# Kernel optimization log

Hardware: AMD Instinct MI355X
Metric: run time of the kernel (lower is better)

Reference implementation:

```python
import jax, jax.numpy as jnp
import numpy as np
from functools import partial

REG = 0.1
NUM_ITERS = 50
EPS_NORM = 1e-8
EPS_SINK = 1e-10


def _cdist(x0, x1):
    # torch.cdist(p=2): pairwise euclidean distance [B,N,N]
    sq0 = jnp.sum(x0 * x0, axis=-1)                     # [B,N]
    sq1 = jnp.sum(x1 * x1, axis=-1)                     # [B,N]
    inner = jnp.einsum('bnd,bmd->bnm', x0, x1)          # [B,N,N]
    d2 = sq0[:, :, None] + sq1[:, None, :] - 2.0 * inner
    return jnp.sqrt(jnp.maximum(d2, 0.0))


def setup_inputs() -> dict:
    key = jax.random.key(0)
    k0, k1 = jax.random.split(key)
    B, N, D = 8, 2048, 64
    x0 = jax.random.normal(k0, (B, N, D), dtype=jnp.float32)
    x1 = jax.random.normal(k1, (B, N, D), dtype=jnp.float32)
    return {"x0": x0, "x1": x1}


def reference(x0, x1):
    B, N, D = x0.shape
    # cost matrix + per-batch max normalization
    C = _cdist(x0, x1)
    C = C / (jnp.max(C, axis=(-2, -1), keepdims=True) + EPS_NORM)
    # Gibbs kernel
    K = jnp.exp(-C / REG)                               # [B,N,N]
    # Sinkhorn fixed-point iterations
    u0 = jnp.full((B, N), 1.0 / N, dtype=K.dtype)
    v0 = jnp.full((B, N), 1.0 / N, dtype=K.dtype)

    def body(i, uv):
        u, v = uv
        u = 1.0 / (jnp.einsum('bij,bj->bi', K, v) + EPS_SINK)
        v = 1.0 / (jnp.einsum('bij,bi->bj', K, u) + EPS_SINK)
        return (u, v)

    u, v = jax.lax.fori_loop(0, NUM_ITERS, body, (u0, v0))
    # transport plan P = diag(u) K diag(v)
    P = u[:, :, None] * K * v[:, None, :]               # [B,N,N]
    # greedy matching: argmax over columns
    matchings = jnp.argmax(P, axis=-1)                  # [B,N] int
    return matchings
```

## Files before the change

kernel.cpp:

```cpp
#include <hip/hip_runtime.h>
#include <hip/hip_bf16.h>
#include <stdint.h>

#define BB 8
#define NN 2048
#define DD 64
#define REGv 0.1f
#define NUM_ITERS 50
#define EPS_NORM 1e-8f
#define EPS_SINK 1e-10f
#define CHUNK 16
#define NBLK (NN / CHUNK)

__global__ void init_k(float* v, unsigned* maxd) {
    int t = blockIdx.x * 256 + threadIdx.x;
    if (t < BB * NN) v[t] = 1.0f / (float)NN;
    if (t < BB) maxd[t] = 0u;
}

__global__ void sq_k(const float* __restrict__ x0, const float* __restrict__ x1,
                     float* __restrict__ sq0, float* __restrict__ sq1) {
    int w = (blockIdx.x * 256 + threadIdx.x) >> 6;
    int lane = threadIdx.x & 63;
    if (w >= 2 * BB * NN) return;
    const float* src = (w < BB * NN) ? x0 : x1;
    int r = (w < BB * NN) ? w : w - BB * NN;
    float val = src[(size_t)r * DD + lane];
    float s = val * val;
    #pragma unroll
    for (int off = 32; off; off >>= 1) s += __shfl_xor(s, off);
    if (lane == 0) ((w < BB * NN) ? sq0 : sq1)[r] = s;
}

template<int WRITE>
__global__ __launch_bounds__(256) void distc_k(const float* __restrict__ x0,
                                               const float* __restrict__ x1,
                                               const float* __restrict__ sq0,
                                               const float* __restrict__ sq1,
                                               float* __restrict__ Kd,
                                               unsigned* __restrict__ maxd) {
    __shared__ float x0s[128 * 68];
    __shared__ float x1t[64 * 68];
    __shared__ float wred[4];
    int bid = blockIdx.x;
    int b = bid >> 9;
    int tile = bid & 511;
    int ti = tile >> 5, tj = tile & 31;
    int i0 = ti * 128, j0 = tj * 64;
    int t = threadIdx.x;

    const float4* g0 = (const float4*)(x0 + ((size_t)b * NN + i0) * DD);
    #pragma unroll
    for (int rep = 0; rep < 8; rep++) {
        int e = rep * 256 + t;
        int row = e >> 4, c4 = e & 15;
        *(float4*)&x0s[row * 68 + c4 * 4] = g0[row * 16 + c4];
    }
    const float4* g1 = (const float4*)(x1 + ((size_t)b * NN + j0) * DD);
    #pragma unroll
    for (int rep = 0; rep < 4; rep++) {
        int e = rep * 256 + t;
        int row = e >> 4, c4 = e & 15;
        float4 a = g1[row * 16 + c4];
        x1t[(c4 * 4 + 0) * 68 + row] = a.x;
        x1t[(c4 * 4 + 1) * 68 + row] = a.y;
        x1t[(c4 * 4 + 2) * 68 + row] = a.z;
        x1t[(c4 * 4 + 3) * 68 + row] = a.w;
    }
    __syncthreads();

    int tx = t & 15, ty = t >> 4;
    float4 acc4[8];
    #pragma unroll
    for (int di = 0; di < 8; di++) acc4[di] = make_float4(0.f, 0.f, 0.f, 0.f);

    #pragma unroll
    for (int k4 = 0; k4 < 16; k4++) {
        float4 b0 = *(const float4*)&x1t[(k4 * 4 + 0) * 68 + tx * 4];
        float4 b1 = *(const float4*)&x1t[(k4 * 4 + 1) * 68 + tx * 4];
        float4 b2 = *(const float4*)&x1t[(k4 * 4 + 2) * 68 + tx * 4];
        float4 b3 = *(const float4*)&x1t[(k4 * 4 + 3) * 68 + tx * 4];
        #pragma unroll
        for (int di = 0; di < 8; di++) {
            float4 a = *(const float4*)&x0s[(ty * 8 + di) * 68 + k4 * 4];
            acc4[di].x += a.x * b0.x + a.y * b1.x + a.z * b2.x + a.w * b3.x;
            acc4[di].y += a.x * b0.y + a.y * b1.y + a.z * b2.y + a.w * b3.y;
            acc4[di].z += a.x * b0.z + a.y * b1.z + a.z * b2.z + a.w * b3.z;
            acc4[di].w += a.x * b0.w + a.y * b1.w + a.z * b2.w + a.w * b3.w;
        }
    }

    int ib = b * NN + i0 + ty * 8;
    float4 s1 = *(const float4*)&sq1[b * NN + j0 + tx * 4];

    if (WRITE) {
        float mv = sqrtf(__uint_as_float(maxd[b])) + EPS_NORM;
        #pragma unroll
        for (int di = 0; di < 8; di++) {
            float s0 = sq0[ib + di];
            float4 o;
            o.x = expf(-((sqrtf(fmaxf(s0 + s1.x - 2.f * acc4[di].x, 0.f)) / mv) / REGv));
            o.y = expf(-((sqrtf(fmaxf(s0 + s1.y - 2.f * acc4[di].y, 0.f)) / mv) / REGv));
            o.z = expf(-((sqrtf(fmaxf(s0 + s1.z - 2.f * acc4[di].z, 0.f)) / mv) / REGv));
            o.w = expf(-((sqrtf(fmaxf(s0 + s1.w - 2.f * acc4[di].w, 0.f)) / mv) / REGv));
            *(float4*)&Kd[(size_t)(ib + di) * NN + j0 + tx * 4] = o;
        }
    } else {
        float lm = 0.0f;
        #pragma unroll
        for (int di = 0; di < 8; di++) {
            float s0 = sq0[ib + di];
            lm = fmaxf(lm, fmaxf(s0 + s1.x - 2.f * acc4[di].x, 0.f));
            lm = fmaxf(lm, fmaxf(s0 + s1.y - 2.f * acc4[di].y, 0.f));
            lm = fmaxf(lm, fmaxf(s0 + s1.z - 2.f * acc4[di].z, 0.f));
            lm = fmaxf(lm, fmaxf(s0 + s1.w - 2.f * acc4[di].w, 0.f));
        }
        #pragma unroll
        for (int off = 32; off; off >>= 1) lm = fmaxf(lm, __shfl_xor(lm, off));
        if ((t & 63) == 0) wred[t >> 6] = lm;
        __syncthreads();
        if (t == 0) {
            float m = fmaxf(fmaxf(wred[0], wred[1]), fmaxf(wred[2], wred[3]));
            atomicMax(&maxd[b], __float_as_uint(m));
        }
    }
}

__global__ __launch_bounds__(512) void sink_k(const float* __restrict__ Kd,
                                              const float* __restrict__ v,
                                              float* __restrict__ u,
                                              float* __restrict__ partial) {
    __shared__ float red[8][CHUNK];
    __shared__ float uu_s[CHUNK];
    int bid = blockIdx.x;
    int b = bid >> 7;
    int chunk = bid & 127;
    int row0 = chunk * CHUNK;
    int t = threadIdx.x;

    float4 vv = ((const float4*)(v + (size_t)b * NN))[t];
    const float4* Kr = (const float4*)(Kd + ((size_t)b * NN + row0) * NN);
    float4 kk[CHUNK];
    #pragma unroll
    for (int r = 0; r < CHUNK; r++) kk[r] = Kr[r * 512 + t];

    float dp[CHUNK];
    #pragma unroll
    for (int r = 0; r < CHUNK; r++)
        dp[r] = kk[r].x * vv.x + kk[r].y * vv.y + kk[r].z * vv.z + kk[r].w * vv.w;
    #pragma unroll
    for (int r = 0; r < CHUNK; r++)
        #pragma unroll
        for (int off = 32; off; off >>= 1) dp[r] += __shfl_xor(dp[r], off);
    int lane = t & 63, w = t >> 6;
    if (lane == 0) {
        #pragma unroll
        for (int r = 0; r < CHUNK; r++) red[w][r] = dp[r];
    }
    __syncthreads();
    if (t < CHUNK) {
        float s = 0.0f;
        #pragma unroll
        for (int c = 0; c < 8; c++) s += red[c][t];
        float uu = 1.0f / (s + EPS_SINK);
        uu_s[t] = uu;
        u[(size_t)b * NN + row0 + t] = uu;
    }
    __syncthreads();

    float4 acc = make_float4(0.f, 0.f, 0.f, 0.f);
    #pragma unroll
    for (int r = 0; r < CHUNK; r++) {
        float uur = uu_s[r];
        acc.x += uur * kk[r].x; acc.y += uur * kk[r].y;
        acc.z += uur * kk[r].z; acc.w += uur * kk[r].w;
    }
    ((float4*)(partial + ((size_t)b * NBLK + chunk) * NN))[t] = acc;
}

__global__ void vred_k(const float* __restrict__ partial, float* __restrict__ v) {
    int j = blockIdx.x * 256 + threadIdx.x;
    int b = j >> 11, jj = j & 2047;
    const float* p = partial + (size_t)b * NBLK * NN + jj;
    float s = 0.0f;
    for (int c = 0; c < NBLK; c++) s += p[(size_t)c * NN];
    v[j] = 1.0f / (s + EPS_SINK);
}

__global__ __launch_bounds__(256) void argmax_k(const float* __restrict__ Kd,
                                                const float* __restrict__ u,
                                                const float* __restrict__ v,
                                                int* __restrict__ out) {
    int w = (blockIdx.x * 256 + threadIdx.x) >> 6;
    int lane = threadIdx.x & 63;
    int b = w >> 11, i = w & 2047;
    float uu = u[(size_t)b * NN + i];
    const float4* Kr = (const float4*)(Kd + ((size_t)b * NN + i) * NN);
    const float4* v4 = (const float4*)(v + (size_t)b * NN);
    float best = -1.0f;
    int bidx = 0;
    for (int it = 0; it < 8; it++) {
        int c4 = it * 64 + lane;
        float4 kk = Kr[c4];
        float4 vv = v4[c4];
        int j = c4 * 4;
        float p0 = (uu * kk.x) * vv.x;
        float p1 = (uu * kk.y) * vv.y;
        float p2 = (uu * kk.z) * vv.z;
        float p3 = (uu * kk.w) * vv.w;
        if (p0 > best) { best = p0; bidx = j; }
        if (p1 > best) { best = p1; bidx = j + 1; }
        if (p2 > best) { best = p2; bidx = j + 2; }
        if (p3 > best) { best = p3; bidx = j + 3; }
    }
    #pragma unroll
    for (int off = 32; off; off >>= 1) {
        float ov = __shfl_xor(best, off);
        int oi = __shfl_xor(bidx, off);
        if (ov > best || (ov == best && oi < bidx)) { best = ov; bidx = oi; }
    }
    if (lane == 0) out[(size_t)b * NN + i] = bidx;
}

extern "C" void kernel_launch(void* const* d_in, const int* in_sizes, int n_in,
                              void* d_out, int out_size, void* d_ws, size_t ws_size,
                              hipStream_t stream) {
    const float* x0 = (const float*)d_in[0];
    const float* x1 = (const float*)d_in[1];
    int* out = (int*)d_out;
    char* ws = (char*)d_ws;

    float* Kd      = (float*)(ws + 0ull);
    float* partial = (float*)(ws + 134217728ull);
    float* u       = (float*)(ws + 142606336ull);
    float* v       = (float*)(ws + 142671872ull);
    float* sq0     = (float*)(ws + 142737408ull);
    float* sq1     = (float*)(ws + 142802944ull);
    unsigned* maxd = (unsigned*)(ws + 142868480ull);

    init_k<<<64, 256, 0, stream>>>(v, maxd);
    sq_k<<<8192, 256, 0, stream>>>(x0, x1, sq0, sq1);
    distc_k<0><<<4096, 256, 0, stream>>>(x0, x1, sq0, sq1, Kd, maxd);
    distc_k<1><<<4096, 256, 0, stream>>>(x0, x1, sq0, sq1, Kd, maxd);
    for (int it = 0; it < NUM_ITERS; ++it) {
        sink_k<<<1024, 512, 0, stream>>>(Kd, v, u, partial);
        vred_k<<<64, 256, 0, stream>>>(partial, v);
    }
    argmax_k<<<4096, 256, 0, stream>>>(Kd, u, v, out);
}
```

Before: 1.661 ms.

## Fuse Sinkhorn loop and argmax into persistent kernel with K held on-chip

Replaces the 100 per-iteration sink/vred launches and the final argmax launch with one persistent kernel of 256 blocks. Each block keeps its 64-row slab of K resident in registers and LDS for all 50 iterations, so K is read from HBM only once instead of once per iteration. Blocks exchange column partial sums through global memory and a software grid barrier. This relies on all 256 blocks being co-resident (512 threads, two blocks per CU); if they are not, the barrier deadlocks. The large register and LDS footprint also limits occupancy.

```diff
diff --git a/kernel.cpp b/kernel.cpp
--- a/kernel.cpp
+++ b/kernel.cpp
@@ -1,5 +1,4 @@
 #include <hip/hip_runtime.h>
-#include <hip/hip_bf16.h>
 #include <stdint.h>
 
 #define BB 8
@@ -9,13 +8,20 @@
 #define NUM_ITERS 50
 #define EPS_NORM 1e-8f
 #define EPS_SINK 1e-10f
-#define CHUNK 16
-#define NBLK (NN / CHUNK)
-
-__global__ void init_k(float* v, unsigned* maxd) {
-    int t = blockIdx.x * 256 + threadIdx.x;
-    if (t < BB * NN) v[t] = 1.0f / (float)NN;
+#define GRID_P 256u
+#define NBAR 128
+
+__device__ __forceinline__ float dot4(float4 a, float4 b) {
+    return a.x * b.x + a.y * b.y + a.z * b.z + a.w * b.w;
+}
+__device__ __forceinline__ float4 fma4(float u, float4 k, float4 s) {
+    s.x += u * k.x; s.y += u * k.y; s.z += u * k.z; s.w += u * k.w; return s;
+}
+
+__global__ void init_k(unsigned* maxd, unsigned* bar) {
+    int t = threadIdx.x;
     if (t < BB) maxd[t] = 0u;
+    if (t < NBAR) bar[t] = 0u;
 }
 
 __global__ void sq_k(const float* __restrict__ x0, const float* __restrict__ x1,
@@ -126,100 +132,180 @@
     }
 }
 
-__global__ __launch_bounds__(512) void sink_k(const float* __restrict__ Kd,
-                                              const float* __restrict__ v,
-                                              float* __restrict__ u,
-                                              float* __restrict__ partial) {
-    __shared__ float red[8][CHUNK];
-    __shared__ float uu_s[CHUNK];
-    int bid = blockIdx.x;
-    int b = bid >> 7;
-    int chunk = bid & 127;
-    int row0 = chunk * CHUNK;
-    int t = threadIdx.x;
-
-    float4 vv = ((const float4*)(v + (size_t)b * NN))[t];
-    const float4* Kr = (const float4*)(Kd + ((size_t)b * NN + row0) * NN);
-    float4 kk[CHUNK];
-    #pragma unroll
-    for (int r = 0; r < CHUNK; r++) kk[r] = Kr[r * 512 + t];
-
-    float dp[CHUNK];
-    #pragma unroll
-    for (int r = 0; r < CHUNK; r++)
-        dp[r] = kk[r].x * vv.x + kk[r].y * vv.y + kk[r].z * vv.z + kk[r].w * vv.w;
-    #pragma unroll
-    for (int r = 0; r < CHUNK; r++)
-        #pragma unroll
-        for (int off = 32; off; off >>= 1) dp[r] += __shfl_xor(dp[r], off);
-    int lane = t & 63, w = t >> 6;
-    if (lane == 0) {
-        #pragma unroll
-        for (int r = 0; r < CHUNK; r++) red[w][r] = dp[r];
-    }
+__device__ __forceinline__ void gbar(unsigned* c, int t) {
     __syncthreads();
-    if (t < CHUNK) {
-        float s = 0.0f;
-        #pragma unroll
-        for (int c = 0; c < 8; c++) s += red[c][t];
-        float uu = 1.0f / (s + EPS_SINK);
-        uu_s[t] = uu;
-        u[(size_t)b * NN + row0 + t] = uu;
+    if (t == 0) {
+        __threadfence();
+        atomicAdd(c, 1u);
+        while (__hip_atomic_load(c, __ATOMIC_RELAXED, __HIP_MEMORY_SCOPE_AGENT) < GRID_P)
+            __builtin_amdgcn_s_sleep(1);
+        __threadfence();
     }
     __syncthreads();
-
-    float4 acc = make_float4(0.f, 0.f, 0.f, 0.f);
-    #pragma unroll
-    for (int r = 0; r < CHUNK; r++) {
-        float uur = uu_s[r];
-        acc.x += uur * kk[r].x; acc.y += uur * kk[r].y;
-        acc.z += uur * kk[r].z; acc.w += uur * kk[r].w;
-    }
-    ((float4*)(partial + ((size_t)b * NBLK + chunk) * NN))[t] = acc;
-}
-
-__global__ void vred_k(const float* __restrict__ partial, float* __restrict__ v) {
-    int j = blockIdx.x * 256 + threadIdx.x;
-    int b = j >> 11, jj = j & 2047;
-    const float* p = partial + (size_t)b * NBLK * NN + jj;
-    float s = 0.0f;
-    for (int c = 0; c < NBLK; c++) s += p[(size_t)c * NN];
-    v[j] = 1.0f / (s + EPS_SINK);
-}
-
-__global__ __launch_bounds__(256) void argmax_k(const float* __restrict__ Kd,
-                                                const float* __restrict__ u,
-                                                const float* __restrict__ v,
-                                                int* __restrict__ out) {
-    int w = (blockIdx.x * 256 + threadIdx.x) >> 6;
-    int lane = threadIdx.x & 63;
-    int b = w >> 11, i = w & 2047;
-    float uu = u[(size_t)b * NN + i];
-    const float4* Kr = (const float4*)(Kd + ((size_t)b * NN + i) * NN);
-    const float4* v4 = (const float4*)(v + (size_t)b * NN);
-    float best = -1.0f;
-    int bidx = 0;
-    for (int it = 0; it < 8; it++) {
-        int c4 = it * 64 + lane;
-        float4 kk = Kr[c4];
-        float4 vv = v4[c4];
-        int j = c4 * 4;
-        float p0 = (uu * kk.x) * vv.x;
-        float p1 = (uu * kk.y) * vv.y;
-        float p2 = (uu * kk.z) * vv.z;
-        float p3 = (uu * kk.w) * vv.w;
-        if (p0 > best) { best = p0; bidx = j; }
-        if (p1 > best) { best = p1; bidx = j + 1; }
-        if (p2 > best) { best = p2; bidx = j + 2; }
-        if (p3 > best) { best = p3; bidx = j + 3; }
-    }
-    #pragma unroll
-    for (int off = 32; off; off >>= 1) {
-        float ov = __shfl_xor(best, off);
-        int oi = __shfl_xor(bidx, off);
-        if (ov > best || (ov == best && oi < bidx)) { best = ov; bidx = oi; }
-    }
-    if (lane == 0) out[(size_t)b * NN + i] = bidx;
+}
+
+__global__ __launch_bounds__(512, 2) void persist_k(const float* __restrict__ Kd,
+                                                    float* __restrict__ partial,
+                                                    float* __restrict__ vglob,
+                                                    unsigned* __restrict__ bar,
+                                                    int* __restrict__ out) {
+    __shared__ float4 Kl4[16 * 512];
+    __shared__ float4 vbuf4[512];
+    __shared__ float4 s0buf[512];
+    __shared__ float4 s1buf[512];
+
+    const int t = threadIdx.x;
+    const int l = t & 63;
+    const int w = t >> 6;
+    const int q = blockIdx.x;
+    const int b = q >> 5;
+    const int g = q & 31;
+
+    const float4* Kg = (const float4*)Kd + (size_t)(b * NN + g * 64 + w * 8) * 512;
+
+    #pragma unroll
+    for (int rr = 0; rr < 2; rr++)
+        #pragma unroll
+        for (int k = 0; k < 8; k++)
+            Kl4[(w * 2 + rr) * 512 + k * 64 + l] = Kg[(size_t)(6 + rr) * 512 + k * 64 + l];
+
+    float4 Kreg[6][8];
+    #pragma unroll
+    for (int r = 0; r < 6; r++)
+        #pragma unroll
+        for (int k = 0; k < 8; k++)
+            Kreg[r][k] = Kg[(size_t)r * 512 + k * 64 + l];
+
+    vbuf4[t] = make_float4(1.0f / NN, 1.0f / NN, 1.0f / NN, 1.0f / NN);
+
+    const int kb6 = (w * 2) * 512 + l;
+    const int kb7 = kb6 + 512;
+
+    float u[8];
+
+    for (int it = 0; it < NUM_ITERS; ++it) {
+        __syncthreads();
+
+        float dp[8] = {0, 0, 0, 0, 0, 0, 0, 0};
+        #pragma unroll
+        for (int k = 0; k < 8; k++) {
+            float4 vk = vbuf4[k * 64 + l];
+            float4 c6 = Kl4[kb6 + k * 64];
+            float4 c7 = Kl4[kb7 + k * 64];
+            #pragma unroll
+            for (int r = 0; r < 6; r++) dp[r] += dot4(Kreg[r][k], vk);
+            dp[6] += dot4(c6, vk);
+            dp[7] += dot4(c7, vk);
+            __builtin_amdgcn_sched_barrier(0);
+        }
+        #pragma unroll
+        for (int r = 0; r < 8; r++) {
+            float s = dp[r];
+            #pragma unroll
+            for (int off = 32; off; off >>= 1) s += __shfl_xor(s, off);
+            u[r] = 1.0f / (s + EPS_SINK);
+        }
+
+        float4 sg[8];
+        #pragma unroll
+        for (int k = 0; k < 8; k++) {
+            float4 c6 = Kl4[kb6 + k * 64];
+            float4 c7 = Kl4[kb7 + k * 64];
+            float4 s = make_float4(0.f, 0.f, 0.f, 0.f);
+            #pragma unroll
+            for (int r = 0; r < 6; r++) s = fma4(u[r], Kreg[r][k], s);
+            s = fma4(u[6], c6, s);
+            s = fma4(u[7], c7, s);
+            sg[k] = s;
+            __builtin_amdgcn_sched_barrier(0);
+        }
+
+        float4* mybuf = (w < 4) ? s0buf : s1buf;
+        const int ws = w & 3;
+        #pragma unroll
+        for (int step = 0; step < 4; step++) {
+            if (ws == step) {
+                #pragma unroll
+                for (int k = 0; k < 8; k++) {
+                    int idx = k * 64 + l;
+                    float4 cur = (step == 0) ? make_float4(0.f, 0.f, 0.f, 0.f) : mybuf[idx];
+                    cur.x += sg[k].x; cur.y += sg[k].y; cur.z += sg[k].z; cur.w += sg[k].w;
+                    mybuf[idx] = cur;
+                }
+            }
+            __syncthreads();
+        }
+
+        {
+            float4 a = s0buf[t], c = s1buf[t];
+            float4 pt = make_float4(a.x + c.x, a.y + c.y, a.z + c.z, a.w + c.w);
+            ((float4*)partial)[(size_t)(b * 32 + g) * 512 + t] = pt;
+        }
+        gbar(&bar[2 * it], t);
+
+        {
+            int c4 = g * 16 + (t & 15);
+            int prow = t >> 4;
+            float4 pv = ((const float4*)partial)[(size_t)(b * 32 + prow) * 512 + c4];
+            #pragma unroll
+            for (int off = 16; off <= 32; off <<= 1) {
+                pv.x += __shfl_xor(pv.x, off);
+                pv.y += __shfl_xor(pv.y, off);
+                pv.z += __shfl_xor(pv.z, off);
+                pv.w += __shfl_xor(pv.w, off);
+            }
+            if (l < 16) s0buf[w * 16 + l] = pv;
+            __syncthreads();
+            if (t < 16) {
+                float4 s = s0buf[t];
+                #pragma unroll
+                for (int ww = 1; ww < 8; ww++) {
+                    float4 o = s0buf[ww * 16 + t];
+                    s.x += o.x; s.y += o.y; s.z += o.z; s.w += o.w;
+                }
+                float4 vv;
+                vv.x = 1.0f / (s.x + EPS_SINK);
+                vv.y = 1.0f / (s.y + EPS_SINK);
+                vv.z = 1.0f / (s.z + EPS_SINK);
+                vv.w = 1.0f / (s.w + EPS_SINK);
+                ((float4*)vglob)[q * 16 + t] = vv;
+            }
+        }
+        gbar(&bar[2 * it + 1], t);
+
+        vbuf4[t] = ((const float4*)vglob)[b * 512 + t];
+    }
+    __syncthreads();
+
+    #pragma unroll
+    for (int r = 0; r < 8; r++) {
+        float best = -1.0f;
+        int bi = 0;
+        #pragma unroll
+        for (int k = 0; k < 8; k++) {
+            float4 vk = vbuf4[k * 64 + l];
+            float4 kr;
+            if (r < 6) kr = Kreg[r][k];
+            else kr = Kl4[(r == 6 ? kb6 : kb7) + k * 64];
+            float4 p;
+            p.x = (u[r] * kr.x) * vk.x;
+            p.y = (u[r] * kr.y) * vk.y;
+            p.z = (u[r] * kr.z) * vk.z;
+            p.w = (u[r] * kr.w) * vk.w;
+            int j0 = k * 256 + l * 4;
+            if (p.x > best) { best = p.x; bi = j0; }
+            if (p.y > best) { best = p.y; bi = j0 + 1; }
+            if (p.z > best) { best = p.z; bi = j0 + 2; }
+            if (p.w > best) { best = p.w; bi = j0 + 3; }
+        }
+        #pragma unroll
+        for (int off = 32; off; off >>= 1) {
+            float ov = __shfl_xor(best, off);
+            int oi = __shfl_xor(bi, off);
+            if (ov > best || (ov == best && oi < bi)) { best = ov; bi = oi; }
+        }
+        if (l == 0) out[b * NN + g * 64 + w * 8 + r] = bi;
+    }
 }
 
 extern "C" void kernel_launch(void* const* d_in, const int* in_sizes, int n_in,
@@ -232,19 +318,15 @@
 
     float* Kd      = (float*)(ws + 0ull);
     float* partial = (float*)(ws + 134217728ull);
-    float* u       = (float*)(ws + 142606336ull);
-    float* v       = (float*)(ws + 142671872ull);
-    float* sq0     = (float*)(ws + 142737408ull);
-    float* sq1     = (float*)(ws + 142802944ull);
-    unsigned* maxd = (unsigned*)(ws + 142868480ull);
-
-    init_k<<<64, 256, 0, stream>>>(v, maxd);
+    float* vglob   = (float*)(ws + 136314880ull);
+    float* sq0     = (float*)(ws + 136380416ull);
+    float* sq1     = (float*)(ws + 136445952ull);
+    unsigned* maxd = (unsigned*)(ws + 136511488ull);
+    unsigned* bar  = (unsigned*)(ws + 136511520ull);
+
+    init_k<<<1, 256, 0, stream>>>(maxd, bar);
     sq_k<<<8192, 256, 0, stream>>>(x0, x1, sq0, sq1);
     distc_k<0><<<4096, 256, 0, stream>>>(x0, x1, sq0, sq1, Kd, maxd);
     distc_k<1><<<4096, 256, 0, stream>>>(x0, x1, sq0, sq1, Kd, maxd);
-    for (int it = 0; it < NUM_ITERS; ++it) {
-        sink_k<<<1024, 512, 0, stream>>>(Kd, v, u, partial);
-        vred_k<<<64, 256, 0, stream>>>(partial, v);
-    }
-    argmax_k<<<4096, 256, 0, stream>>>(Kd, u, v, out);
-}
+    persist_k<<<256, 512, 0, stream>>>(Kd, partial, vglob, bar, out);
+}
```

New measurement: 3.227 ms. 1.94x slower.
